# Performance work log

Hardware: AMD Instinct MI355X
Metric: run time of the kernel (lower is better)

## Reference

```python
import jax, jax.numpy as jnp
import numpy as np

N_NODES = 100000
N_EDGES = 1600000
D_IN, D_HID, D_OUT = 64, 64, 32


def _glorot(key, shape):
    fan_in = shape[0]
    return jax.random.normal(key, shape, dtype=jnp.float32) / np.sqrt(fan_in)


def setup_inputs() -> dict:
    key = jax.random.key(0)
    ks = jax.random.split(key, 12)
    x = jax.random.normal(ks[0], (N_NODES, D_IN), dtype=jnp.float32)
    edge_index = jax.random.randint(ks[1], (2, N_EDGES), 0, N_NODES, dtype=jnp.int32)
    dims = [(D_IN, D_HID), (D_HID, D_HID), (D_HID, D_OUT)]
    params = {}
    for i, (din, dout) in enumerate(dims):
        params[f"Wl{i}"] = _glorot(ks[2 + 3 * i], (din, dout))
        params[f"Wr{i}"] = _glorot(ks[3 + 3 * i], (din, dout))
        params[f"b{i}"] = jnp.zeros((dout,), dtype=jnp.float32)
    return {"x": x, "edge_index": edge_index, **params}


def _sage_conv(h, src, dst, deg_inv, Wl, Wr, b):
    # mean-aggregate neighbor features: gather from src, scatter-sum to dst
    msg_sum = jax.ops.segment_sum(h[src], dst, num_segments=N_NODES)  # [N, F]
    mean = msg_sum * deg_inv[:, None]
    # lin_l(mean) + bias + lin_r(h)  (PyG SAGEConv: bias lives in lin_l)
    return mean @ Wl + b + h @ Wr


def reference(x, edge_index, Wl0, Wr0, b0, Wl1, Wr1, b1, Wl2, Wr2, b2):
    src, dst = edge_index[0], edge_index[1]
    deg = jax.ops.segment_sum(jnp.ones((N_EDGES,), x.dtype), dst, num_segments=N_NODES)
    deg_inv = 1.0 / jnp.maximum(deg, 1.0)  # mean with clamp for isolated nodes
    h = jax.nn.elu(_sage_conv(x, src, dst, deg_inv, Wl0, Wr0, b0))
    h = jax.nn.elu(_sage_conv(h, src, dst, deg_inv, Wl1, Wr1, b1))
    return _sage_conv(h, src, dst, deg_inv, Wl2, Wr2, b2)
```

## Files before the change

### kernel.cpp

```cpp
#include <hip/hip_runtime.h>
#include <cstdint>
#include <cstddef>


constexpr int SBW = 256;
constexpr int LOGSBW = 8;
constexpr int CAPS = 4608;
constexpr int CHK = 2048;

typedef __attribute__((ext_vector_type(8))) short s16x8;
typedef __attribute__((ext_vector_type(4))) float f32x4;

__device__ inline unsigned short f2bf(float f) {
  unsigned u = __builtin_bit_cast(unsigned, f);
  u += 0x7FFFu + ((u >> 16) & 1u);
  return (unsigned short)(u >> 16);
}
__device__ inline float bf2f(unsigned short b) {
  unsigned u = ((unsigned)b) << 16;
  return __builtin_bit_cast(float, u);
}


__global__ __launch_bounds__(256) void bin_coarse(const int* __restrict__ src,
                                                  const int* __restrict__ dst,
                                                  int* __restrict__ bcur,
                                                  unsigned int* __restrict__ coarse,
                                                  int NSB, int E) {
  __shared__ int h[512];
  __shared__ unsigned ed[CHK];
  __shared__ short sb[CHK];
  const int tid = threadIdx.x;
  for (int i = tid; i < NSB; i += 256) h[i] = 0;
  __syncthreads();
  const int e0 = blockIdx.x * CHK;
  const int e1 = min(E, e0 + CHK);
  for (int e = e0 + tid; e < e1; e += 256) {
    int d = dst[e];
    int s = src[e];
    int b = d >> LOGSBW;
    ed[e - e0] = (unsigned)s | ((unsigned)(d & (SBW - 1)) << 17);
    sb[e - e0] = (short)b;
    atomicAdd(&h[b], 1);
  }
  __syncthreads();
  for (int i = tid; i < NSB; i += 256) {
    int c = h[i];
    h[i] = c ? (i * CAPS + atomicAdd(&bcur[i], c)) : 0;
  }
  __syncthreads();
  const int n = e1 - e0;
  for (int k = tid; k < n; k += 256) {
    int b = sb[k];
    int pos = atomicAdd(&h[b], 1);
    if (pos < (b + 1) * CAPS)
      coarse[pos] = ed[k];
  }
}


__global__ __launch_bounds__(256) void super_csr(const unsigned int* __restrict__ coarse,
                                                 const int* __restrict__ bcur,
                                                 int* __restrict__ rowstart,
                                                 int* __restrict__ degarr,
                                                 float* __restrict__ deg_inv,
                                                 int* __restrict__ colidx,
                                                 int N) {
  __shared__ int cnt[SBW];
  __shared__ int sc[SBW];
  __shared__ int cur[SBW];
  const int b = blockIdx.x;
  const int tid = threadIdx.x;
  cnt[tid] = 0;
  __syncthreads();
  const int ec = min(bcur[b], CAPS);
  const int base = b * CAPS;
  for (int e = tid; e < ec; e += 256)
    atomicAdd(&cnt[coarse[base + e] >> 17], 1);
  __syncthreads();
  int v = cnt[tid];
  sc[tid] = v;
  __syncthreads();
  for (int off = 1; off < SBW; off <<= 1) {
    int y = sc[tid];
    if (tid >= off) y += sc[tid - off];
    __syncthreads();
    sc[tid] = y;
    __syncthreads();
  }
  int ex = sc[tid] - v;
  cur[tid] = ex;
  int gn = b * SBW + tid;
  if (gn < N) {
    rowstart[gn] = base + ex;
    degarr[gn] = v;
    deg_inv[gn] = 1.0f / (float)(v > 1 ? v : 1);
  }
  __syncthreads();
  for (int e = tid; e < ec; e += 256) {
    unsigned p = coarse[base + e];
    int dl = (int)(p >> 17);
    int s = (int)(p & 0x1FFFFu);
    int l = atomicAdd(&cur[dl], 1);
    colidx[base + l] = s;
  }
}


__global__ __launch_bounds__(256) void cvt_bf16(const float* __restrict__ x,
                                                unsigned short* __restrict__ y,
                                                int n) {
  int i = (blockIdx.x * 256 + threadIdx.x) * 4;
  if (i < n) {
    float4 v = *(const float4*)&x[i];
    ushort4 o;
    o.x = f2bf(v.x); o.y = f2bf(v.y); o.z = f2bf(v.z); o.w = f2bf(v.w);
    *(ushort4*)&y[i] = o;
  }
}


template <int DOUT>
__global__ __launch_bounds__(256) void gemm_mfma(const unsigned short* __restrict__ Hm,
                                                 const float* __restrict__ Wl,
                                                 const float* __restrict__ Wr,
                                                 const float* __restrict__ bias,
                                                 unsigned short* __restrict__ t_out,
                                                 float* __restrict__ r_out, int N) {
  constexpr int NTT = DOUT / 16;
  constexpr int SK = 72;
  __shared__ short Wt[2 * DOUT * SK];

  const int tid = threadIdx.x;
  for (int idx = tid; idx < 64 * DOUT; idx += 256) {
    int k = idx / DOUT, c = idx % DOUT;
    Wt[c * SK + k] = (short)f2bf(Wl[idx]);
    Wt[(c + DOUT) * SK + k] = (short)f2bf(Wr[idx]);
  }
  __syncthreads();

  const int wv = tid >> 6, lane = tid & 63;
  const int q = lane >> 4, m = lane & 15;
  const int row = blockIdx.x * 64 + wv * 16 + m;
  const int rowc = row < N ? row : N - 1;
  const s16x8 a0 = *(const s16x8*)&Hm[(size_t)rowc * 64 + q * 8];
  const s16x8 a1 = *(const s16x8*)&Hm[(size_t)rowc * 64 + 32 + q * 8];

  f32x4 acc[2 * NTT];
#pragma unroll
  for (int c = 0; c < 2 * NTT; ++c) acc[c] = (f32x4){0.f, 0.f, 0.f, 0.f};

#pragma unroll
  for (int c = 0; c < 2 * NTT; ++c) {
    const short* wp = &Wt[(c * 16 + m) * SK];
    s16x8 b0 = *(const s16x8*)&wp[q * 8];
    s16x8 b1 = *(const s16x8*)&wp[32 + q * 8];
    acc[c] = __builtin_amdgcn_mfma_f32_16x16x32_bf16(a0, b0, acc[c], 0, 0, 0);
    acc[c] = __builtin_amdgcn_mfma_f32_16x16x32_bf16(a1, b1, acc[c], 0, 0, 0);
  }

  const int orow = blockIdx.x * 64 + wv * 16 + q * 4;
#pragma unroll
  for (int c = 0; c < NTT; ++c) {
#pragma unroll
    for (int i = 0; i < 4; ++i) {
      int r_ = orow + i;
      if (r_ < N) t_out[(size_t)r_ * DOUT + c * 16 + m] = f2bf(acc[c][i]);
    }
  }
#pragma unroll
  for (int c = 0; c < NTT; ++c) {
    float bv = bias[c * 16 + m];
#pragma unroll
    for (int i = 0; i < 4; ++i) {
      int r_ = orow + i;
      if (r_ < N) r_out[(size_t)r_ * DOUT + c * 16 + m] = acc[NTT + c][i] + bv;
    }
  }
}


template <int DOUT, bool DO_ELU, bool BF16OUT>
__global__ __launch_bounds__(256) void gather_mean(const uint2* __restrict__ t,
                                                   const float* r,
                                                   const float* __restrict__ deg_inv,
                                                   const int* __restrict__ rowstart,
                                                   const int* __restrict__ degarr,
                                                   const int* __restrict__ colidx,
                                                   void* out, int N) {
  constexpr int L = DOUT / 4;
  int node = blockIdx.x * (256 / L) + threadIdx.x / L;
  int lane = threadIdx.x & (L - 1);
  if (node >= N) return;
  int b = rowstart[node];
  int e = b + degarr[node];
  float s0 = 0.f, s1 = 0.f, s2 = 0.f, s3 = 0.f;
  int i = b;
  for (; i + 8 <= e; i += 8) {
    uint2 v[8];
#pragma unroll
    for (int j = 0; j < 8; ++j)
      v[j] = t[(size_t)colidx[i + j] * L + lane];
#pragma unroll
    for (int j = 0; j < 8; ++j) {
      s0 += bf2f((unsigned short)(v[j].x & 0xFFFFu));
      s1 += bf2f((unsigned short)(v[j].x >> 16));
      s2 += bf2f((unsigned short)(v[j].y & 0xFFFFu));
      s3 += bf2f((unsigned short)(v[j].y >> 16));
    }
  }
  for (; i < e; ++i) {
    uint2 v = t[(size_t)colidx[i] * L + lane];
    s0 += bf2f((unsigned short)(v.x & 0xFFFFu));
    s1 += bf2f((unsigned short)(v.x >> 16));
    s2 += bf2f((unsigned short)(v.y & 0xFFFFu));
    s3 += bf2f((unsigned short)(v.y >> 16));
  }
  float dv = deg_inv[node];
  float4 rv = *(const float4*)&r[(size_t)node * DOUT + 4 * lane];
  float a0 = s0 * dv + rv.x;
  float a1 = s1 * dv + rv.y;
  float a2 = s2 * dv + rv.z;
  float a3 = s3 * dv + rv.w;
  if (DO_ELU) {
    a0 = a0 > 0.f ? a0 : (expf(a0) - 1.f);
    a1 = a1 > 0.f ? a1 : (expf(a1) - 1.f);
    a2 = a2 > 0.f ? a2 : (expf(a2) - 1.f);
    a3 = a3 > 0.f ? a3 : (expf(a3) - 1.f);
  }
  if (BF16OUT) {
    ushort4 hv;
    hv.x = f2bf(a0); hv.y = f2bf(a1); hv.z = f2bf(a2); hv.w = f2bf(a3);
    *(ushort4*)&((unsigned short*)out)[(size_t)node * DOUT + 4 * lane] = hv;
  } else {
    *(float4*)&((float*)out)[(size_t)node * DOUT + 4 * lane] =
        make_float4(a0, a1, a2, a3);
  }
}


extern "C" void kernel_launch(void* const* d_in, const int* in_sizes, int n_in,
                              void* d_out, int out_size, void* d_ws, size_t ws_size,
                              hipStream_t stream) {
  const float* x   = (const float*)d_in[0];
  const int*   ei  = (const int*)d_in[1];
  const float* Wl0 = (const float*)d_in[2];
  const float* Wr0 = (const float*)d_in[3];
  const float* b0  = (const float*)d_in[4];
  const float* Wl1 = (const float*)d_in[5];
  const float* Wr1 = (const float*)d_in[6];
  const float* b1  = (const float*)d_in[7];
  const float* Wl2 = (const float*)d_in[8];
  const float* Wr2 = (const float*)d_in[9];
  const float* b2  = (const float*)d_in[10];
  float* out = (float*)d_out;

  const int N = in_sizes[0] / 64;
  const int E = in_sizes[1] / 2;
  const int* srcv = ei;
  const int* dstv = ei + E;
  const int NSB = (N + SBW - 1) >> LOGSBW;

  auto al = [](size_t v) { return (v + 255) & ~(size_t)255; };
  char* w = (char*)d_ws;
  size_t oBcur = 0;
  size_t oRow  = oBcur + al(4 * (size_t)NSB);
  size_t oDeg  = oRow + al(4 * (size_t)N);
  size_t oDinv = oDeg + al(4 * (size_t)N);
  size_t oBin  = oDinv + al(4 * (size_t)N);
  size_t oCol  = oBin + al(4 * (size_t)NSB * CAPS);
  size_t oP    = oCol + al(4 * (size_t)NSB * CAPS);
  size_t oX    = oP + al(2 * (size_t)N * 64);
  size_t oR    = oX + al(2 * (size_t)N * 64);

  int*            bcur     = (int*)(w + oBcur);
  int*            rowstart = (int*)(w + oRow);
  int*            degarr   = (int*)(w + oDeg);
  float*          deg_inv  = (float*)(w + oDinv);
  unsigned*       coarse   = (unsigned*)(w + oBin);
  int*            colidx   = (int*)(w + oCol);
  unsigned short* P        = (unsigned short*)(w + oP);
  unsigned short* X        = (unsigned short*)(w + oX);
  float*          R        = (float*)(w + oR);

  hipMemsetAsync(bcur, 0, (size_t)NSB * 4, stream);

  int bbl = (E + CHK - 1) / CHK;
  bin_coarse<<<bbl, 256, 0, stream>>>(srcv, dstv, bcur, coarse, NSB, E);
  super_csr<<<NSB, 256, 0, stream>>>(coarse, bcur, rowstart, degarr, deg_inv, colidx, N);
  cvt_bf16<<<(N * 64 / 4 + 255) / 256, 256, 0, stream>>>(x, X, N * 64);

  int gb = (N + 63) / 64;
  gemm_mfma<64><<<gb, 256, 0, stream>>>(X, Wl0, Wr0, b0, P, R, N);
  gather_mean<64, true, true><<<(N + 15) / 16, 256, 0, stream>>>(
      (const uint2*)P, R, deg_inv, rowstart, degarr, colidx, X, N);
  gemm_mfma<64><<<gb, 256, 0, stream>>>(X, Wl1, Wr1, b1, P, R, N);
  gather_mean<64, true, true><<<(N + 15) / 16, 256, 0, stream>>>(
      (const uint2*)P, R, deg_inv, rowstart, degarr, colidx, X, N);
  gemm_mfma<32><<<gb, 256, 0, stream>>>(X, Wl2, Wr2, b2, P, out, N);
  gather_mean<32, false, false><<<(N + 31) / 32, 256, 0, stream>>>(
      (const uint2*)P, out, deg_inv, rowstart, degarr, colidx, out, N);
}
```

Before: 283.4 us.

## Fuse gather-mean with next layer GEMM and fold bf16 conversion into first GEMM

Removes the separate fp32-to-bf16 conversion kernel by converting x inside the first GEMM. Fuses each layer's neighbour gather, mean, residual and ELU with the next layer's MFMA GEMM, keeping the activated tile in shared memory. This avoids writing the hidden activations to global memory and launching extra kernels. Ping-pong P/R buffers are added, and the fused kernel needs more shared memory with a block barrier between the gather and GEMM phases, which may reduce occupancy for the latency-bound gather.

```diff
diff --git a/kernel.cpp b/kernel.cpp
--- a/kernel.cpp
+++ b/kernel.cpp
@@ -107,26 +107,13 @@
 }
 
 
-__global__ __launch_bounds__(256) void cvt_bf16(const float* __restrict__ x,
-                                                unsigned short* __restrict__ y,
-                                                int n) {
-  int i = (blockIdx.x * 256 + threadIdx.x) * 4;
-  if (i < n) {
-    float4 v = *(const float4*)&x[i];
-    ushort4 o;
-    o.x = f2bf(v.x); o.y = f2bf(v.y); o.z = f2bf(v.z); o.w = f2bf(v.w);
-    *(ushort4*)&y[i] = o;
-  }
-}
-
-
-template <int DOUT>
-__global__ __launch_bounds__(256) void gemm_mfma(const unsigned short* __restrict__ Hm,
-                                                 const float* __restrict__ Wl,
-                                                 const float* __restrict__ Wr,
-                                                 const float* __restrict__ bias,
-                                                 unsigned short* __restrict__ t_out,
-                                                 float* __restrict__ r_out, int N) {
+__global__ __launch_bounds__(256) void gemm0_mfma(const float* __restrict__ x,
+                                                  const float* __restrict__ Wl,
+                                                  const float* __restrict__ Wr,
+                                                  const float* __restrict__ bias,
+                                                  unsigned short* __restrict__ t_out,
+                                                  float* __restrict__ r_out, int N) {
+  constexpr int DOUT = 64;
   constexpr int NTT = DOUT / 16;
   constexpr int SK = 72;
   __shared__ short Wt[2 * DOUT * SK];
@@ -143,13 +130,24 @@
   const int q = lane >> 4, m = lane & 15;
   const int row = blockIdx.x * 64 + wv * 16 + m;
   const int rowc = row < N ? row : N - 1;
-  const s16x8 a0 = *(const s16x8*)&Hm[(size_t)rowc * 64 + q * 8];
-  const s16x8 a1 = *(const s16x8*)&Hm[(size_t)rowc * 64 + 32 + q * 8];
+  const float* xp = &x[(size_t)rowc * 64];
+  float4 f0 = *(const float4*)&xp[q * 8];
+  float4 f1 = *(const float4*)&xp[q * 8 + 4];
+  float4 f2 = *(const float4*)&xp[32 + q * 8];
+  float4 f3 = *(const float4*)&xp[32 + q * 8 + 4];
+  s16x8 a0, a1;
+  a0[0] = (short)f2bf(f0.x); a0[1] = (short)f2bf(f0.y);
+  a0[2] = (short)f2bf(f0.z); a0[3] = (short)f2bf(f0.w);
+  a0[4] = (short)f2bf(f1.x); a0[5] = (short)f2bf(f1.y);
+  a0[6] = (short)f2bf(f1.z); a0[7] = (short)f2bf(f1.w);
+  a1[0] = (short)f2bf(f2.x); a1[1] = (short)f2bf(f2.y);
+  a1[2] = (short)f2bf(f2.z); a1[3] = (short)f2bf(f2.w);
+  a1[4] = (short)f2bf(f3.x); a1[5] = (short)f2bf(f3.y);
+  a1[6] = (short)f2bf(f3.z); a1[7] = (short)f2bf(f3.w);
 
   f32x4 acc[2 * NTT];
 #pragma unroll
   for (int c = 0; c < 2 * NTT; ++c) acc[c] = (f32x4){0.f, 0.f, 0.f, 0.f};
-
 #pragma unroll
   for (int c = 0; c < 2 * NTT; ++c) {
     const short* wp = &Wt[(c * 16 + m) * SK];
@@ -180,16 +178,121 @@
 }
 
 
-template <int DOUT, bool DO_ELU, bool BF16OUT>
-__global__ __launch_bounds__(256) void gather_mean(const uint2* __restrict__ t,
-                                                   const float* r,
-                                                   const float* __restrict__ deg_inv,
-                                                   const int* __restrict__ rowstart,
-                                                   const int* __restrict__ degarr,
-                                                   const int* __restrict__ colidx,
-                                                   void* out, int N) {
-  constexpr int L = DOUT / 4;
-  int node = blockIdx.x * (256 / L) + threadIdx.x / L;
+template <int DOUT>
+__global__ __launch_bounds__(256) void fused_gather_gemm(
+    const uint2* __restrict__ t_in, const float* __restrict__ r_in,
+    const float* __restrict__ deg_inv, const int* __restrict__ rowstart,
+    const int* __restrict__ degarr, const int* __restrict__ colidx,
+    const float* __restrict__ Wl, const float* __restrict__ Wr,
+    const float* __restrict__ bias,
+    unsigned short* __restrict__ t_out, float* __restrict__ r_out, int N) {
+  constexpr int NTT = DOUT / 16;
+  constexpr int SK = 72;
+  __shared__ short Wt[2 * DOUT * SK];
+  __shared__ short hs[64 * SK];
+
+  const int tid = threadIdx.x;
+  for (int idx = tid; idx < 64 * DOUT; idx += 256) {
+    int k = idx / DOUT, c = idx % DOUT;
+    Wt[c * SK + k] = (short)f2bf(Wl[idx]);
+    Wt[(c + DOUT) * SK + k] = (short)f2bf(Wr[idx]);
+  }
+
+  const int sg = tid >> 4, lane = tid & 15;
+  const int node0 = blockIdx.x * 64;
+#pragma unroll
+  for (int p = 0; p < 4; ++p) {
+    int nl = p * 16 + sg;
+    int node = node0 + nl;
+    if (node < N) {
+      int b = rowstart[node];
+      int e = b + degarr[node];
+      float s0 = 0.f, s1 = 0.f, s2 = 0.f, s3 = 0.f;
+      int i = b;
+      for (; i + 8 <= e; i += 8) {
+        uint2 v[8];
+#pragma unroll
+        for (int j = 0; j < 8; ++j)
+          v[j] = t_in[(size_t)colidx[i + j] * 16 + lane];
+#pragma unroll
+        for (int j = 0; j < 8; ++j) {
+          s0 += bf2f((unsigned short)(v[j].x & 0xFFFFu));
+          s1 += bf2f((unsigned short)(v[j].x >> 16));
+          s2 += bf2f((unsigned short)(v[j].y & 0xFFFFu));
+          s3 += bf2f((unsigned short)(v[j].y >> 16));
+        }
+      }
+      for (; i < e; ++i) {
+        uint2 v = t_in[(size_t)colidx[i] * 16 + lane];
+        s0 += bf2f((unsigned short)(v.x & 0xFFFFu));
+        s1 += bf2f((unsigned short)(v.x >> 16));
+        s2 += bf2f((unsigned short)(v.y & 0xFFFFu));
+        s3 += bf2f((unsigned short)(v.y >> 16));
+      }
+      float dv = deg_inv[node];
+      float4 rv = *(const float4*)&r_in[(size_t)node * 64 + 4 * lane];
+      float a0 = s0 * dv + rv.x;
+      float a1 = s1 * dv + rv.y;
+      float a2 = s2 * dv + rv.z;
+      float a3 = s3 * dv + rv.w;
+      a0 = a0 > 0.f ? a0 : (expf(a0) - 1.f);
+      a1 = a1 > 0.f ? a1 : (expf(a1) - 1.f);
+      a2 = a2 > 0.f ? a2 : (expf(a2) - 1.f);
+      a3 = a3 > 0.f ? a3 : (expf(a3) - 1.f);
+      ushort4 hv;
+      hv.x = f2bf(a0); hv.y = f2bf(a1); hv.z = f2bf(a2); hv.w = f2bf(a3);
+      *(ushort4*)&hs[nl * SK + 4 * lane] = hv;
+    }
+  }
+  __syncthreads();
+
+  const int wv = tid >> 6, l64 = tid & 63;
+  const int q = l64 >> 4, m = l64 & 15;
+  const s16x8 a0 = *(const s16x8*)&hs[(wv * 16 + m) * SK + q * 8];
+  const s16x8 a1 = *(const s16x8*)&hs[(wv * 16 + m) * SK + 32 + q * 8];
+
+  f32x4 acc[2 * NTT];
+#pragma unroll
+  for (int c = 0; c < 2 * NTT; ++c) acc[c] = (f32x4){0.f, 0.f, 0.f, 0.f};
+#pragma unroll
+  for (int c = 0; c < 2 * NTT; ++c) {
+    const short* wp = &Wt[(c * 16 + m) * SK];
+    s16x8 b0 = *(const s16x8*)&wp[q * 8];
+    s16x8 b1 = *(const s16x8*)&wp[32 + q * 8];
+    acc[c] = __builtin_amdgcn_mfma_f32_16x16x32_bf16(a0, b0, acc[c], 0, 0, 0);
+    acc[c] = __builtin_amdgcn_mfma_f32_16x16x32_bf16(a1, b1, acc[c], 0, 0, 0);
+  }
+
+  const int orow = blockIdx.x * 64 + wv * 16 + q * 4;
+#pragma unroll
+  for (int c = 0; c < NTT; ++c) {
+#pragma unroll
+    for (int i = 0; i < 4; ++i) {
+      int r_ = orow + i;
+      if (r_ < N) t_out[(size_t)r_ * DOUT + c * 16 + m] = f2bf(acc[c][i]);
+    }
+  }
+#pragma unroll
+  for (int c = 0; c < NTT; ++c) {
+    float bv = bias[c * 16 + m];
+#pragma unroll
+    for (int i = 0; i < 4; ++i) {
+      int r_ = orow + i;
+      if (r_ < N) r_out[(size_t)r_ * DOUT + c * 16 + m] = acc[NTT + c][i] + bv;
+    }
+  }
+}
+
+
+__global__ __launch_bounds__(256) void gather_out(const uint2* __restrict__ t,
+                                                  const float* __restrict__ r,
+                                                  const float* __restrict__ deg_inv,
+                                                  const int* __restrict__ rowstart,
+                                                  const int* __restrict__ degarr,
+                                                  const int* __restrict__ colidx,
+                                                  float* __restrict__ out, int N) {
+  constexpr int L = 8;
+  int node = blockIdx.x * 32 + threadIdx.x / L;
   int lane = threadIdx.x & (L - 1);
   if (node >= N) return;
   int b = rowstart[node];
@@ -217,25 +320,9 @@
     s3 += bf2f((unsigned short)(v.y >> 16));
   }
   float dv = deg_inv[node];
-  float4 rv = *(const float4*)&r[(size_t)node * DOUT + 4 * lane];
-  float a0 = s0 * dv + rv.x;
-  float a1 = s1 * dv + rv.y;
-  float a2 = s2 * dv + rv.z;
-  float a3 = s3 * dv + rv.w;
-  if (DO_ELU) {
-    a0 = a0 > 0.f ? a0 : (expf(a0) - 1.f);
-    a1 = a1 > 0.f ? a1 : (expf(a1) - 1.f);
-    a2 = a2 > 0.f ? a2 : (expf(a2) - 1.f);
-    a3 = a3 > 0.f ? a3 : (expf(a3) - 1.f);
-  }
-  if (BF16OUT) {
-    ushort4 hv;
-    hv.x = f2bf(a0); hv.y = f2bf(a1); hv.z = f2bf(a2); hv.w = f2bf(a3);
-    *(ushort4*)&((unsigned short*)out)[(size_t)node * DOUT + 4 * lane] = hv;
-  } else {
-    *(float4*)&((float*)out)[(size_t)node * DOUT + 4 * lane] =
-        make_float4(a0, a1, a2, a3);
-  }
+  float4 rv = *(const float4*)&r[(size_t)node * 32 + 4 * lane];
+  *(float4*)&out[(size_t)node * 32 + 4 * lane] =
+      make_float4(s0 * dv + rv.x, s1 * dv + rv.y, s2 * dv + rv.z, s3 * dv + rv.w);
 }
 
 
@@ -269,9 +356,10 @@
   size_t oDinv = oDeg + al(4 * (size_t)N);
   size_t oBin  = oDinv + al(4 * (size_t)N);
   size_t oCol  = oBin + al(4 * (size_t)NSB * CAPS);
-  size_t oP    = oCol + al(4 * (size_t)NSB * CAPS);
-  size_t oX    = oP + al(2 * (size_t)N * 64);
-  size_t oR    = oX + al(2 * (size_t)N * 64);
+  size_t oP0   = oCol + al(4 * (size_t)NSB * CAPS);
+  size_t oP1   = oP0 + al(2 * (size_t)N * 64);
+  size_t oR0   = oP1 + al(2 * (size_t)N * 64);
+  size_t oR1   = oR0 + al(4 * (size_t)N * 64);
 
   int*            bcur     = (int*)(w + oBcur);
   int*            rowstart = (int*)(w + oRow);
@@ -279,25 +367,25 @@
   float*          deg_inv  = (float*)(w + oDinv);
   unsigned*       coarse   = (unsigned*)(w + oBin);
   int*            colidx   = (int*)(w + oCol);
-  unsigned short* P        = (unsigned short*)(w + oP);
-  unsigned short* X        = (unsigned short*)(w + oX);
-  float*          R        = (float*)(w + oR);
+  unsigned short* P0       = (unsigned short*)(w + oP0);
+  unsigned short* P1       = (unsigned short*)(w + oP1);
+  float*          R0       = (float*)(w + oR0);
+  float*          R1       = (float*)(w + oR1);
 
   hipMemsetAsync(bcur, 0, (size_t)NSB * 4, stream);
 
   int bbl = (E + CHK - 1) / CHK;
   bin_coarse<<<bbl, 256, 0, stream>>>(srcv, dstv, bcur, coarse, NSB, E);
   super_csr<<<NSB, 256, 0, stream>>>(coarse, bcur, rowstart, degarr, deg_inv, colidx, N);
-  cvt_bf16<<<(N * 64 / 4 + 255) / 256, 256, 0, stream>>>(x, X, N * 64);
 
   int gb = (N + 63) / 64;
-  gemm_mfma<64><<<gb, 256, 0, stream>>>(X, Wl0, Wr0, b0, P, R, N);
-  gather_mean<64, true, true><<<(N + 15) / 16, 256, 0, stream>>>(
-      (const uint2*)P, R, deg_inv, rowstart, degarr, colidx, X, N);
-  gemm_mfma<64><<<gb, 256, 0, stream>>>(X, Wl1, Wr1, b1, P, R, N);
-  gather_mean<64, true, true><<<(N + 15) / 16, 256, 0, stream>>>(
-      (const uint2*)P, R, deg_inv, rowstart, degarr, colidx, X, N);
-  gemm_mfma<32><<<gb, 256, 0, stream>>>(X, Wl2, Wr2, b2, P, out, N);
-  gather_mean<32, false, false><<<(N + 31) / 32, 256, 0, stream>>>(
-      (const uint2*)P, out, deg_inv, rowstart, degarr, colidx, out, N);
-}
+  gemm0_mfma<<<gb, 256, 0, stream>>>(x, Wl0, Wr0, b0, P0, R0, N);
+  fused_gather_gemm<64><<<gb, 256, 0, stream>>>(
+      (const uint2*)P0, R0, deg_inv, rowstart, degarr, colidx,
+      Wl1, Wr1, b1, P1, R1, N);
+  fused_gather_gemm<32><<<gb, 256, 0, stream>>>(
+      (const uint2*)P1, R1, deg_inv, rowstart, degarr, colidx,
+      Wl2, Wr2, b2, P0, R0, N);
+  gather_out<<<(N + 31) / 32, 256, 0, stream>>>(
+      (const uint2*)P0, R0, deg_inv, rowstart, degarr, colidx, out, N);
+}
```

After: 294.5 us. 1.04x slower.

## Prestage swizzled bf16 weights once and fuse input conversion into first GEMM

Applied to the files above, without the earlier changes.

A small kernel converts all six weight matrices to bf16 once, in the exact per-lane MFMA fragment order, so every GEMM block no longer rebuilds a transposed copy in shared memory or waits on a barrier. The first-layer GEMM now reads the fp32 input directly and converts it in registers, which removes the separate conversion kernel and its bf16 round trip through memory. The last layer writes its root term to a scratch buffer instead of aliasing the output, and restrict qualifiers are added to the gather kernel. In exchange there is one extra tiny launch, and weights are read from global memory or cache instead of LDS.

```diff
diff --git a/kernel.cpp b/kernel.cpp
--- a/kernel.cpp
+++ b/kernel.cpp
@@ -107,38 +107,114 @@
 }
 
 
-__global__ __launch_bounds__(256) void cvt_bf16(const float* __restrict__ x,
-                                                unsigned short* __restrict__ y,
-                                                int n) {
-  int i = (blockIdx.x * 256 + threadIdx.x) * 4;
-  if (i < n) {
-    float4 v = *(const float4*)&x[i];
-    ushort4 o;
-    o.x = f2bf(v.x); o.y = f2bf(v.y); o.z = f2bf(v.z); o.w = f2bf(v.w);
-    *(ushort4*)&y[i] = o;
+__global__ __launch_bounds__(256) void stage_w(const float* __restrict__ Wl0,
+                                               const float* __restrict__ Wr0,
+                                               const float* __restrict__ Wl1,
+                                               const float* __restrict__ Wr1,
+                                               const float* __restrict__ Wl2,
+                                               const float* __restrict__ Wr2,
+                                               unsigned short* __restrict__ Wsw) {
+  int g = blockIdx.x * 256 + threadIdx.x;
+  if (g >= 10240) return;
+  int s = g * 2;
+  int layer, off;
+  if (s < 8192)       { layer = 0; off = 0; }
+  else if (s < 16384) { layer = 1; off = 8192; }
+  else                { layer = 2; off = 16384; }
+  int t = s - off;
+  int D = (layer == 2) ? 32 : 64;
+  int NTT = D / 16;
+  int tt = t >> 10;
+  int rem = t & 1023;
+  int plane = rem >> 9;
+  int rem2 = rem & 511;
+  int lane = rem2 >> 3;
+  int j = rem2 & 7;
+  int q = lane >> 4, m = lane & 15;
+  int k = plane * 32 + q * 8 + j;
+  const float* W;
+  int c;
+  if (tt < NTT) {
+    c = tt;
+    W = (layer == 0) ? Wl0 : (layer == 1) ? Wl1 : Wl2;
+  } else {
+    c = tt - NTT;
+    W = (layer == 0) ? Wr0 : (layer == 1) ? Wr1 : Wr2;
+  }
+  int col = c * 16 + m;
+  unsigned lo = f2bf(W[k * D + col]);
+  unsigned hi = f2bf(W[(k + 1) * D + col]);
+  *(unsigned*)&Wsw[s] = lo | (hi << 16);
+}
+
+
+__global__ __launch_bounds__(256) void gemm0_mfma(const float* __restrict__ x,
+                                                  const unsigned short* __restrict__ Wf,
+                                                  const float* __restrict__ bias,
+                                                  unsigned short* __restrict__ t_out,
+                                                  float* __restrict__ r_out, int N) {
+  constexpr int DOUT = 64;
+  constexpr int NTT = 4;
+  const int tid = threadIdx.x;
+  const int wv = tid >> 6, lane = tid & 63;
+  const int q = lane >> 4, m = lane & 15;
+  const int row = blockIdx.x * 64 + wv * 16 + m;
+  const int rowc = row < N ? row : N - 1;
+  const float* xp = &x[(size_t)rowc * 64];
+  float4 f0 = *(const float4*)&xp[q * 8];
+  float4 f1 = *(const float4*)&xp[q * 8 + 4];
+  float4 f2 = *(const float4*)&xp[32 + q * 8];
+  float4 f3 = *(const float4*)&xp[32 + q * 8 + 4];
+  s16x8 a0, a1;
+  a0[0] = (short)f2bf(f0.x); a0[1] = (short)f2bf(f0.y);
+  a0[2] = (short)f2bf(f0.z); a0[3] = (short)f2bf(f0.w);
+  a0[4] = (short)f2bf(f1.x); a0[5] = (short)f2bf(f1.y);
+  a0[6] = (short)f2bf(f1.z); a0[7] = (short)f2bf(f1.w);
+  a1[0] = (short)f2bf(f2.x); a1[1] = (short)f2bf(f2.y);
+  a1[2] = (short)f2bf(f2.z); a1[3] = (short)f2bf(f2.w);
+  a1[4] = (short)f2bf(f3.x); a1[5] = (short)f2bf(f3.y);
+  a1[6] = (short)f2bf(f3.z); a1[7] = (short)f2bf(f3.w);
+
+  f32x4 acc[2 * NTT];
+#pragma unroll
+  for (int c = 0; c < 2 * NTT; ++c) acc[c] = (f32x4){0.f, 0.f, 0.f, 0.f};
+#pragma unroll
+  for (int c = 0; c < 2 * NTT; ++c) {
+    s16x8 b0 = *(const s16x8*)&Wf[(c * 2 + 0) * 512 + lane * 8];
+    s16x8 b1 = *(const s16x8*)&Wf[(c * 2 + 1) * 512 + lane * 8];
+    acc[c] = __builtin_amdgcn_mfma_f32_16x16x32_bf16(a0, b0, acc[c], 0, 0, 0);
+    acc[c] = __builtin_amdgcn_mfma_f32_16x16x32_bf16(a1, b1, acc[c], 0, 0, 0);
+  }
+
+  const int orow = blockIdx.x * 64 + wv * 16 + q * 4;
+#pragma unroll
+  for (int c = 0; c < NTT; ++c) {
+#pragma unroll
+    for (int i = 0; i < 4; ++i) {
+      int r_ = orow + i;
+      if (r_ < N) t_out[(size_t)r_ * DOUT + c * 16 + m] = f2bf(acc[c][i]);
+    }
+  }
+#pragma unroll
+  for (int c = 0; c < NTT; ++c) {
+    float bv = bias[c * 16 + m];
+#pragma unroll
+    for (int i = 0; i < 4; ++i) {
+      int r_ = orow + i;
+      if (r_ < N) r_out[(size_t)r_ * DOUT + c * 16 + m] = acc[NTT + c][i] + bv;
+    }
   }
 }
 
 
 template <int DOUT>
 __global__ __launch_bounds__(256) void gemm_mfma(const unsigned short* __restrict__ Hm,
-                                                 const float* __restrict__ Wl,
-                                                 const float* __restrict__ Wr,
+                                                 const unsigned short* __restrict__ Wf,
                                                  const float* __restrict__ bias,
                                                  unsigned short* __restrict__ t_out,
                                                  float* __restrict__ r_out, int N) {
   constexpr int NTT = DOUT / 16;
-  constexpr int SK = 72;
-  __shared__ short Wt[2 * DOUT * SK];
-
   const int tid = threadIdx.x;
-  for (int idx = tid; idx < 64 * DOUT; idx += 256) {
-    int k = idx / DOUT, c = idx % DOUT;
-    Wt[c * SK + k] = (short)f2bf(Wl[idx]);
-    Wt[(c + DOUT) * SK + k] = (short)f2bf(Wr[idx]);
-  }
-  __syncthreads();
-
   const int wv = tid >> 6, lane = tid & 63;
   const int q = lane >> 4, m = lane & 15;
   const int row = blockIdx.x * 64 + wv * 16 + m;
@@ -149,12 +225,10 @@
   f32x4 acc[2 * NTT];
 #pragma unroll
   for (int c = 0; c < 2 * NTT; ++c) acc[c] = (f32x4){0.f, 0.f, 0.f, 0.f};
-
 #pragma unroll
   for (int c = 0; c < 2 * NTT; ++c) {
-    const short* wp = &Wt[(c * 16 + m) * SK];
-    s16x8 b0 = *(const s16x8*)&wp[q * 8];
-    s16x8 b1 = *(const s16x8*)&wp[32 + q * 8];
+    s16x8 b0 = *(const s16x8*)&Wf[(c * 2 + 0) * 512 + lane * 8];
+    s16x8 b1 = *(const s16x8*)&Wf[(c * 2 + 1) * 512 + lane * 8];
     acc[c] = __builtin_amdgcn_mfma_f32_16x16x32_bf16(a0, b0, acc[c], 0, 0, 0);
     acc[c] = __builtin_amdgcn_mfma_f32_16x16x32_bf16(a1, b1, acc[c], 0, 0, 0);
   }
@@ -182,12 +256,12 @@
 
 template <int DOUT, bool DO_ELU, bool BF16OUT>
 __global__ __launch_bounds__(256) void gather_mean(const uint2* __restrict__ t,
-                                                   const float* r,
+                                                   const float* __restrict__ r,
                                                    const float* __restrict__ deg_inv,
                                                    const int* __restrict__ rowstart,
                                                    const int* __restrict__ degarr,
                                                    const int* __restrict__ colidx,
-                                                   void* out, int N) {
+                                                   void* __restrict__ out, int N) {
   constexpr int L = DOUT / 4;
   int node = blockIdx.x * (256 / L) + threadIdx.x / L;
   int lane = threadIdx.x & (L - 1);
@@ -267,7 +341,8 @@
   size_t oRow  = oBcur + al(4 * (size_t)NSB);
   size_t oDeg  = oRow + al(4 * (size_t)N);
   size_t oDinv = oDeg + al(4 * (size_t)N);
-  size_t oBin  = oDinv + al(4 * (size_t)N);
+  size_t oWsw  = oDinv + al(4 * (size_t)N);
+  size_t oBin  = oWsw + al(2 * 20480);
   size_t oCol  = oBin + al(4 * (size_t)NSB * CAPS);
   size_t oP    = oCol + al(4 * (size_t)NSB * CAPS);
   size_t oX    = oP + al(2 * (size_t)N * 64);
@@ -277,6 +352,7 @@
   int*            rowstart = (int*)(w + oRow);
   int*            degarr   = (int*)(w + oDeg);
   float*          deg_inv  = (float*)(w + oDinv);
+  unsigned short* Wsw      = (unsigned short*)(w + oWsw);
   unsigned*       coarse   = (unsigned*)(w + oBin);
   int*            colidx   = (int*)(w + oCol);
   unsigned short* P        = (unsigned short*)(w + oP);
@@ -285,19 +361,19 @@
 
   hipMemsetAsync(bcur, 0, (size_t)NSB * 4, stream);
 
+  stage_w<<<40, 256, 0, stream>>>(Wl0, Wr0, Wl1, Wr1, Wl2, Wr2, Wsw);
   int bbl = (E + CHK - 1) / CHK;
   bin_coarse<<<bbl, 256, 0, stream>>>(srcv, dstv, bcur, coarse, NSB, E);
   super_csr<<<NSB, 256, 0, stream>>>(coarse, bcur, rowstart, degarr, deg_inv, colidx, N);
-  cvt_bf16<<<(N * 64 / 4 + 255) / 256, 256, 0, stream>>>(x, X, N * 64);
 
   int gb = (N + 63) / 64;
-  gemm_mfma<64><<<gb, 256, 0, stream>>>(X, Wl0, Wr0, b0, P, R, N);
+  gemm0_mfma<<<gb, 256, 0, stream>>>(x, Wsw, b0, P, R, N);
   gather_mean<64, true, true><<<(N + 15) / 16, 256, 0, stream>>>(
       (const uint2*)P, R, deg_inv, rowstart, degarr, colidx, X, N);
-  gemm_mfma<64><<<gb, 256, 0, stream>>>(X, Wl1, Wr1, b1, P, R, N);
+  gemm_mfma<64><<<gb, 256, 0, stream>>>(X, Wsw + 8192, b1, P, R, N);
   gather_mean<64, true, true><<<(N + 15) / 16, 256, 0, stream>>>(
       (const uint2*)P, R, deg_inv, rowstart, degarr, colidx, X, N);
-  gemm_mfma<32><<<gb, 256, 0, stream>>>(X, Wl2, Wr2, b2, P, out, N);
+  gemm_mfma<32><<<gb, 256, 0, stream>>>(X, Wsw + 16384, b2, P, R, N);
   gather_mean<32, false, false><<<(N + 31) / 32, 256, 0, stream>>>(
-      (const uint2*)P, out, deg_inv, rowstart, degarr, colidx, out, N);
-}
+      (const uint2*)P, R, deg_inv, rowstart, degarr, colidx, out, N);
+}
```

New measurement: 285.8 us. Within noise of the previous version (+0.8%).
